# Optimization experiments

Hardware: AMD Instinct MI355X
Metric: run time of the kernel (lower is better)

## Reference

```python
import jax, jax.numpy as jnp
import numpy as np

N = 16384            # number of input vectors
CODEBOOK_SIZE = 8192  # M
DIM = 256             # dim_feature
BETA = 0.25           # commitment_weight


def setup_inputs() -> dict:
    key = jax.random.key(0)
    kx, ke = jax.random.split(key)
    x = jax.random.normal(kx, (N, DIM), dtype=jnp.float32)
    # kaiming-uniform-style init for the codebook
    bound = float(np.sqrt(3.0 / DIM))
    embeddings = jax.random.uniform(ke, (CODEBOOK_SIZE, DIM), dtype=jnp.float32,
                                    minval=-bound, maxval=bound)
    return {"x": x, "embeddings": embeddings}


def reference(x, embeddings):
    # l2_dist: sqrt(sum((x_i - e_j)^2)) computed via the GEMM expansion
    x2 = jnp.sum(x * x, axis=1, keepdims=True)               # (N, 1)
    e2 = jnp.sum(embeddings * embeddings, axis=1)            # (M,)
    d2 = x2 + e2[None, :] - 2.0 * (x @ embeddings.T)         # (N, M)
    dist = jnp.sqrt(jnp.maximum(d2, 0.0))
    # deterministic gumbel_sample path (training eval / stochastic=False):
    # argmax of logits = -dist  <=>  argmin of dist
    ind = jnp.argmin(dist, axis=1)                           # (N,)
    quantized = embeddings[ind]                              # one_hot @ embeddings
    # commitment loss: beta * ||x_q - sg(x)||^2 (docstring)
    commit_loss = BETA * jnp.mean((quantized - jax.lax.stop_gradient(x)) ** 2)
    # straight-through estimator
    quantized_st = x + jax.lax.stop_gradient(quantized - x)
    # perplexity from per-code counts (one-hot scatter)
    counts = jnp.zeros((CODEBOOK_SIZE,), jnp.float32).at[ind].add(1.0)
    probs = counts / counts.sum()
    perplexity = jnp.exp(-jnp.sum(probs * jnp.log(probs + 1e-10)))
    return quantized_st, ind, commit_loss, perplexity
```

## Files before the change

kernel.cpp:

```cpp
#include <hip/hip_runtime.h>
#include <stdint.h>


#define N_VEC 16384
#define M_CODES 8192
#define DIM 256
#define BETA 0.25f

#define NSLICE 4
#define SLICE_CODES 2048
#define BM 256
#define BN 256
#define NPART 8

#define XSLOT 32768
#define ESLOT 32768
#define EBASE (3 * XSLOT)
#define LDS_TOTAL (3 * XSLOT + 2 * ESLOT)
#define NSTEPS 64

typedef __attribute__((ext_vector_type(4))) float f32x4;
typedef __attribute__((ext_vector_type(8))) __bf16 bf16x8;

__device__ __forceinline__ void gll16(const void* g, const void* lds_p) {
    __builtin_amdgcn_global_load_lds(
        (const __attribute__((address_space(1))) uint32_t*)(uintptr_t)g,
        (__attribute__((address_space(3))) uint32_t*)(uint32_t)(uintptr_t)lds_p,
        16, 0, 0);
}
#define SB0() __builtin_amdgcn_sched_barrier(0)

__device__ __forceinline__ ushort f2bf(float f) {
    uint32_t u = __float_as_uint(f);
    return (ushort)((u + 0x7FFFu + ((u >> 16) & 1u)) >> 16);
}
__device__ __forceinline__ float bf2f(ushort h) {
    return __uint_as_float(((uint32_t)h) << 16);
}

__global__ __launch_bounds__(256) void prep_kernel(
    const float* __restrict__ x, const float* __restrict__ emb,
    ushort* __restrict__ xh, ushort* __restrict__ xl,
    ushort* __restrict__ eh, ushort* __restrict__ el,
    float* __restrict__ e2, unsigned* __restrict__ counts,
    float* __restrict__ loss_acc) {
    if (blockIdx.x < 8) {
        int4 z = {0, 0, 0, 0};
        ((int4*)counts)[blockIdx.x * 256 + threadIdx.x] = z;
        if (blockIdx.x == 0 && threadIdx.x == 0) *loss_acc = 0.0f;
    }
    const int wave = threadIdx.x >> 6;
    const int lane = threadIdx.x & 63;
    const int row = blockIdx.x * 4 + wave;

    const float* src;
    ushort* ph;
    ushort* pl;
    bool is_e;
    int er = row - N_VEC;
    if (row < N_VEC) {
        src = x + (size_t)row * DIM;
        ph = xh + (size_t)row * DIM;
        pl = xl + (size_t)row * DIM;
        is_e = false;
    } else {
        src = emb + (size_t)er * DIM;
        ph = eh + (size_t)er * DIM;
        pl = el + (size_t)er * DIM;
        is_e = true;
    }
    float4 v = *(const float4*)(src + lane * 4);
    ushort h0 = f2bf(v.x), h1 = f2bf(v.y), h2 = f2bf(v.z), h3 = f2bf(v.w);
    ushort l0 = f2bf(v.x - bf2f(h0)), l1 = f2bf(v.y - bf2f(h1));
    ushort l2 = f2bf(v.z - bf2f(h2)), l3 = f2bf(v.w - bf2f(h3));
    *(ushort4*)(ph + lane * 4) = make_ushort4(h0, h1, h2, h3);
    *(ushort4*)(pl + lane * 4) = make_ushort4(l0, l1, l2, l3);
    if (is_e) {
        float s = v.x * v.x + v.y * v.y + v.z * v.z + v.w * v.w;
        #pragma unroll
        for (int off = 32; off; off >>= 1) s += __shfl_xor(s, off);
        if (lane == 0) e2[er] = s;
    }
}

__global__ __launch_bounds__(512, 1) void vq_mfma_kernel(
    const ushort* __restrict__ xh, const ushort* __restrict__ xl,
    const ushort* __restrict__ eh, const ushort* __restrict__ el,
    const float* __restrict__ e2g, unsigned long long* __restrict__ partials) {
    extern __shared__ char lds[];

    const int t = threadIdx.x;
    const int lane = t & 63;
    const int wv = t >> 6;
    const int lane15 = lane & 15;
    const int l16 = lane >> 4;

    const int rt = blockIdx.x & 63;
    const int slice = blockIdx.x >> 6;
    const int row0 = rt * BM;
    const int cslice0 = slice * SLICE_CODES;

    const int wr0 = (wv & 3) * 64;
    const int wch = wv >> 2;

    const int swz = ((l16 ^ (lane15 >> 1)) & 3) << 4;
    const int byteA0 = (wr0 + lane15) * 64 + swz;
    const int byteB0 = (wch * 128 + lane15) * 64 + swz;

    const int s0 = wv * 128 + lane;
    const int s1 = s0 + 64;
    const int r0s = s0 >> 2, r1s = s1 >> 2;
    const int c0s = ((s0 & 3) ^ ((s0 >> 3) & 3)) << 3;
    const int c1s = ((s1 & 3) ^ ((s1 >> 3) & 3)) << 3;

    const ushort* pxh_a = xh + (size_t)(row0 + r0s) * DIM + c0s;
    const ushort* pxh_b = xh + (size_t)(row0 + r1s) * DIM + c1s;
    const ushort* pxl_a = xl + (size_t)(row0 + r0s) * DIM + c0s;
    const ushort* pxl_b = xl + (size_t)(row0 + r1s) * DIM + c1s;
    const ushort* peh_a = eh + (size_t)(cslice0 + r0s) * DIM + c0s;
    const ushort* peh_b = eh + (size_t)(cslice0 + r1s) * DIM + c1s;
    const ushort* pel_a = el + (size_t)(cslice0 + r0s) * DIM + c0s;
    const ushort* pel_b = el + (size_t)(cslice0 + r1s) * DIM + c1s;
    const int wdst = wv * 2048;

    auto stage_X = [&](int slot, int s) {
        char* b = lds + slot * XSLOT + wdst;
        const int xo = (s & 7) * 32;
        gll16(pxh_a + xo, b);
        gll16(pxh_b + xo, b + 1024);
        gll16(pxl_a + xo, b + 16384);
        gll16(pxl_b + xo, b + 16384 + 1024);
    };
    auto stage_E = [&](int slot, int s) {
        char* b = lds + EBASE + slot * ESLOT + wdst;
        const size_t eo = ((size_t)(s >> 3) << 16) + (s & 7) * 32;
        gll16(peh_a + eo, b);
        gll16(peh_b + eo, b + 1024);
        gll16(pel_a + eo, b + 16384);
        gll16(pel_b + eo, b + 16384 + 1024);
    };

    float best[16];
    int bidx[16];
    #pragma unroll
    for (int s = 0; s < 16; ++s) { best[s] = __uint_as_float(0x7f800000u); bidx[s] = 0; }

    f32x4 acc[4][8];
    #pragma unroll
    for (int fi = 0; fi < 4; ++fi)
        #pragma unroll
        for (int fj = 0; fj < 8; ++fj) acc[fi][fj] = (f32x4){0.f, 0.f, 0.f, 0.f};

    float e2r[8];

    stage_X(0, 0); SB0();
    stage_E(0, 0); SB0();
    stage_X(1, 1); SB0();

    int xsl = 0;
    for (int s = 0; s < NSTEPS; ++s) {
        if (s == NSTEPS - 1) {
            asm volatile("s_waitcnt vmcnt(0)" ::: "memory");
        } else {
            asm volatile("s_waitcnt vmcnt(4)" ::: "memory");
        }
        __builtin_amdgcn_s_barrier();
        SB0();
        if ((s & 7) == 0) {
            const int ct = s >> 3;
            const int cb = cslice0 + ct * BN + wch * 128 + lane15;
            #pragma unroll
            for (int fj = 0; fj < 8; ++fj) e2r[fj] = e2g[cb + fj * 16];
            SB0();
        }
        if (s + 1 < NSTEPS) { stage_E((s + 1) & 1, s + 1); SB0(); }
        if (s + 2 < NSTEPS) { stage_X((xsl >= 1) ? xsl - 1 : 2, s + 2); SB0(); }

        const char* lbX = lds + xsl * XSLOT;
        const char* lbE = lds + EBASE + (s & 1) * ESLOT;
        bf16x8 ah[4], alo[4];
        #pragma unroll
        for (int f = 0; f < 4; ++f) {
            ah[f] = *(const bf16x8*)(lbX + byteA0 + f * 1024);
            alo[f] = *(const bf16x8*)(lbX + 16384 + byteA0 + f * 1024);
        }
        __builtin_amdgcn_s_setprio(1);
        #pragma unroll
        for (int fj = 0; fj < 8; ++fj) {
            bf16x8 bh = *(const bf16x8*)(lbE + byteB0 + fj * 1024);
            bf16x8 blo = *(const bf16x8*)(lbE + 16384 + byteB0 + fj * 1024);
            #pragma unroll
            for (int fi = 0; fi < 4; ++fi)
                acc[fi][fj] = __builtin_amdgcn_mfma_f32_16x16x32_bf16(
                    ah[fi], bh, acc[fi][fj], 0, 0, 0);
            #pragma unroll
            for (int fi = 0; fi < 4; ++fi)
                acc[fi][fj] = __builtin_amdgcn_mfma_f32_16x16x32_bf16(
                    ah[fi], blo, acc[fi][fj], 0, 0, 0);
            #pragma unroll
            for (int fi = 0; fi < 4; ++fi)
                acc[fi][fj] = __builtin_amdgcn_mfma_f32_16x16x32_bf16(
                    alo[fi], bh, acc[fi][fj], 0, 0, 0);
        }
        __builtin_amdgcn_s_setprio(0);
        xsl = (xsl == 2) ? 0 : xsl + 1;

        if ((s & 7) == 7) {
            const int ct = s >> 3;
            const int cb = cslice0 + ct * BN + wch * 128 + lane15;
            #pragma unroll
            for (int fj = 0; fj < 8; ++fj) {
                const int c = cb + fj * 16;
                #pragma unroll
                for (int fi = 0; fi < 4; ++fi)
                    #pragma unroll
                    for (int r = 0; r < 4; ++r) {
                        float sc = e2r[fj] - 2.0f * acc[fi][fj][r];
                        const int slot = fi * 4 + r;
                        if (sc < best[slot]) { best[slot] = sc; bidx[slot] = c; }
                    }
            }
            #pragma unroll
            for (int fi = 0; fi < 4; ++fi)
                #pragma unroll
                for (int fj = 0; fj < 8; ++fj)
                    acc[fi][fj] = (f32x4){0.f, 0.f, 0.f, 0.f};
        }
    }

    #pragma unroll
    for (int slot = 0; slot < 16; ++slot) {
        float v = best[slot];
        int ix = bidx[slot];
        #pragma unroll
        for (int off = 1; off < 16; off <<= 1) {
            float v2 = __shfl_xor(v, off);
            int ix2 = __shfl_xor(ix, off);
            if (v2 < v || (v2 == v && ix2 < ix)) { v = v2; ix = ix2; }
        }
        if (lane15 == 0) {
            int fi = slot >> 2, r = slot & 3;
            int row = row0 + wr0 + fi * 16 + l16 * 4 + r;
            uint32_t u = __float_as_uint(v);
            uint32_t ord = (u & 0x80000000u) ? ~u : (u | 0x80000000u);
            partials[(size_t)(slice * 2 + wch) * N_VEC + row] =
                ((unsigned long long)ord << 32) | (unsigned)ix;
        }
    }
}

__global__ __launch_bounds__(256) void finish_kernel(
    const float* __restrict__ x, const float* __restrict__ emb,
    const unsigned long long* __restrict__ partials,
    float* __restrict__ out_ind, float* __restrict__ out_q,
    unsigned* __restrict__ counts, float* __restrict__ loss_acc) {
    __shared__ float partial[4];
    const int wave = threadIdx.x >> 6;
    const int lane = threadIdx.x & 63;
    const int row = blockIdx.x * 4 + wave;

    unsigned long long m = ~0ull;
    if (lane < NPART) m = partials[(size_t)lane * N_VEC + row];
    #pragma unroll
    for (int off = 1; off < NPART; off <<= 1) {
        unsigned long long v = __shfl_xor(m, off);
        if (v < m) m = v;
    }
    m = __shfl(m, 0);
    const int ix = (int)(unsigned)(m & 0xFFFFFFFFull);

    float4 q = *(const float4*)(emb + (size_t)ix * DIM + lane * 4);
    float4 xv = *(const float4*)(x + (size_t)row * DIM + lane * 4);
    *(float4*)(out_q + (size_t)row * DIM + lane * 4) = q;
    float dx = q.x - xv.x, dy = q.y - xv.y, dz = q.z - xv.z, dw = q.w - xv.w;
    float s = dx * dx + dy * dy + dz * dz + dw * dw;
    #pragma unroll
    for (int off = 32; off; off >>= 1) s += __shfl_xor(s, off);
    if (lane == 0) {
        out_ind[row] = (float)ix;
        atomicAdd(&counts[ix], 1u);
        partial[wave] = s;
    }
    __syncthreads();
    if (threadIdx.x == 0)
        atomicAdd(loss_acc, partial[0] + partial[1] + partial[2] + partial[3]);
}

__global__ __launch_bounds__(256) void finalize_kernel(
    const unsigned* __restrict__ counts, const float* __restrict__ loss_acc,
    float* __restrict__ out_scalars) {
    __shared__ float red[256];
    float h = 0.0f;
    for (int c = threadIdx.x; c < M_CODES; c += 256) {
        float p = (float)counts[c] * (1.0f / (float)N_VEC);
        h += p * logf(p + 1e-10f);
    }
    red[threadIdx.x] = h;
    __syncthreads();
    for (int s = 128; s; s >>= 1) {
        if (threadIdx.x < s) red[threadIdx.x] += red[threadIdx.x + s];
        __syncthreads();
    }
    if (threadIdx.x == 0) {
        out_scalars[0] = BETA * loss_acc[0] / (float)(N_VEC * DIM);
        out_scalars[1] = expf(-red[0]);
    }
}

extern "C" void kernel_launch(void* const* d_in, const int* in_sizes, int n_in,
                              void* d_out, int out_size, void* d_ws, size_t ws_size,
                              hipStream_t stream) {
    const float* x = (const float*)d_in[0];
    const float* emb = (const float*)d_in[1];

    float* out = (float*)d_out;
    float* out_q = out;
    float* out_ind = out + (size_t)N_VEC * DIM;
    float* out_scalars = out_ind + N_VEC;

    ushort* xh = (ushort*)out;
    ushort* xl = xh + (size_t)N_VEC * DIM;

    char* wp = (char*)d_ws;
    ushort* eh = (ushort*)wp;  wp += (size_t)M_CODES * DIM * 2;
    ushort* el = (ushort*)wp;  wp += (size_t)M_CODES * DIM * 2;
    float* e2 = (float*)wp;    wp += (size_t)M_CODES * 4;
    unsigned long long* partials = (unsigned long long*)wp;
    wp += (size_t)NPART * N_VEC * 8;
    unsigned* counts = (unsigned*)wp; wp += (size_t)M_CODES * 4;
    float* loss_acc = (float*)wp;

    prep_kernel<<<(N_VEC + M_CODES) / 4, 256, 0, stream>>>(x, emb, xh, xl, eh, el,
                                                           e2, counts, loss_acc);

    hipFuncSetAttribute((const void*)vq_mfma_kernel,
                        hipFuncAttributeMaxDynamicSharedMemorySize, LDS_TOTAL);
    vq_mfma_kernel<<<(N_VEC / BM) * NSLICE, 512, LDS_TOTAL, stream>>>(
        xh, xl, eh, el, e2, partials);

    finish_kernel<<<N_VEC / 4, 256, 0, stream>>>(x, emb, partials, out_ind, out_q,
                                                 counts, loss_acc);
    finalize_kernel<<<1, 256, 0, stream>>>(counts, loss_acc, out_scalars);
}
```

Baseline: 240.5 us.

## Shrink GEMM tiles to 128x128 with 256-thread blocks and simple double buffering

Reduces the block tile from 256x256 with 8 waves to 128x128 with 4 waves, and allows two blocks per CU. The separate triple-buffered X and double-buffered E staging becomes one combined double buffer, and each step now waits for all loads to finish. Smaller tiles cut LDS use and register pressure to allow more occupancy. In exchange, each loaded byte feeds fewer MFMAs, global traffic roughly doubles, and load latency is less well hidden because of the vmcnt(0) wait.

```diff
diff --git a/kernel.cpp b/kernel.cpp
--- a/kernel.cpp
+++ b/kernel.cpp
@@ -9,15 +9,13 @@
 
 #define NSLICE 4
 #define SLICE_CODES 2048
-#define BM 256
-#define BN 256
+#define BM 128
+#define BN 128
 #define NPART 8
 
-#define XSLOT 32768
-#define ESLOT 32768
-#define EBASE (3 * XSLOT)
-#define LDS_TOTAL (3 * XSLOT + 2 * ESLOT)
-#define NSTEPS 64
+#define BUFBYTES 32768
+#define LDS_TOTAL (2 * BUFBYTES)
+#define NSTEPS 128
 
 typedef __attribute__((ext_vector_type(4))) float f32x4;
 typedef __attribute__((ext_vector_type(8))) __bf16 bf16x8;
@@ -83,7 +81,7 @@
     }
 }
 
-__global__ __launch_bounds__(512, 1) void vq_mfma_kernel(
+__global__ __launch_bounds__(256, 2) void vq_mfma_kernel(
     const ushort* __restrict__ xh, const ushort* __restrict__ xl,
     const ushort* __restrict__ eh, const ushort* __restrict__ el,
     const float* __restrict__ e2g, unsigned long long* __restrict__ partials) {
@@ -95,17 +93,17 @@
     const int lane15 = lane & 15;
     const int l16 = lane >> 4;
 
-    const int rt = blockIdx.x & 63;
-    const int slice = blockIdx.x >> 6;
+    const int rt = blockIdx.x & 127;
+    const int slice = blockIdx.x >> 7;
     const int row0 = rt * BM;
     const int cslice0 = slice * SLICE_CODES;
 
-    const int wr0 = (wv & 3) * 64;
-    const int wch = wv >> 2;
+    const int wr0 = (wv & 1) * 64;
+    const int wch = wv >> 1;
 
     const int swz = ((l16 ^ (lane15 >> 1)) & 3) << 4;
     const int byteA0 = (wr0 + lane15) * 64 + swz;
-    const int byteB0 = (wch * 128 + lane15) * 64 + swz;
+    const int byteB0 = (wch * 64 + lane15) * 64 + swz;
 
     const int s0 = wv * 128 + lane;
     const int s1 = s0 + 64;
@@ -123,21 +121,18 @@
     const ushort* pel_b = el + (size_t)(cslice0 + r1s) * DIM + c1s;
     const int wdst = wv * 2048;
 
-    auto stage_X = [&](int slot, int s) {
-        char* b = lds + slot * XSLOT + wdst;
+    auto stage = [&](int bufOff, int s) {
+        char* b = lds + bufOff + wdst;
         const int xo = (s & 7) * 32;
+        const size_t eo = ((size_t)(s >> 3) << 15) + (s & 7) * 32;
         gll16(pxh_a + xo, b);
         gll16(pxh_b + xo, b + 1024);
-        gll16(pxl_a + xo, b + 16384);
-        gll16(pxl_b + xo, b + 16384 + 1024);
-    };
-    auto stage_E = [&](int slot, int s) {
-        char* b = lds + EBASE + slot * ESLOT + wdst;
-        const size_t eo = ((size_t)(s >> 3) << 16) + (s & 7) * 32;
-        gll16(peh_a + eo, b);
-        gll16(peh_b + eo, b + 1024);
-        gll16(pel_a + eo, b + 16384);
-        gll16(pel_b + eo, b + 16384 + 1024);
+        gll16(pxl_a + xo, b + 8192);
+        gll16(pxl_b + xo, b + 8192 + 1024);
+        gll16(peh_a + eo, b + 16384);
+        gll16(peh_b + eo, b + 16384 + 1024);
+        gll16(pel_a + eo, b + 24576);
+        gll16(pel_b + eo, b + 24576 + 1024);
     };
 
     float best[16];
@@ -145,50 +140,40 @@
     #pragma unroll
     for (int s = 0; s < 16; ++s) { best[s] = __uint_as_float(0x7f800000u); bidx[s] = 0; }
 
-    f32x4 acc[4][8];
+    f32x4 acc[4][4];
     #pragma unroll
     for (int fi = 0; fi < 4; ++fi)
         #pragma unroll
-        for (int fj = 0; fj < 8; ++fj) acc[fi][fj] = (f32x4){0.f, 0.f, 0.f, 0.f};
-
-    float e2r[8];
-
-    stage_X(0, 0); SB0();
-    stage_E(0, 0); SB0();
-    stage_X(1, 1); SB0();
-
-    int xsl = 0;
+        for (int fj = 0; fj < 4; ++fj) acc[fi][fj] = (f32x4){0.f, 0.f, 0.f, 0.f};
+
+    float e2r[4];
+
+    stage(0, 0); SB0();
+
     for (int s = 0; s < NSTEPS; ++s) {
-        if (s == NSTEPS - 1) {
-            asm volatile("s_waitcnt vmcnt(0)" ::: "memory");
-        } else {
-            asm volatile("s_waitcnt vmcnt(4)" ::: "memory");
-        }
+        asm volatile("s_waitcnt vmcnt(0)" ::: "memory");
         __builtin_amdgcn_s_barrier();
         SB0();
+        if (s + 1 < NSTEPS) { stage(((s + 1) & 1) * BUFBYTES, s + 1); SB0(); }
         if ((s & 7) == 0) {
-            const int ct = s >> 3;
-            const int cb = cslice0 + ct * BN + wch * 128 + lane15;
-            #pragma unroll
-            for (int fj = 0; fj < 8; ++fj) e2r[fj] = e2g[cb + fj * 16];
+            const int cb = cslice0 + (s >> 3) * BN + wch * 64 + lane15;
+            #pragma unroll
+            for (int fj = 0; fj < 4; ++fj) e2r[fj] = e2g[cb + fj * 16];
             SB0();
         }
-        if (s + 1 < NSTEPS) { stage_E((s + 1) & 1, s + 1); SB0(); }
-        if (s + 2 < NSTEPS) { stage_X((xsl >= 1) ? xsl - 1 : 2, s + 2); SB0(); }
-
-        const char* lbX = lds + xsl * XSLOT;
-        const char* lbE = lds + EBASE + (s & 1) * ESLOT;
+
+        const char* lb = lds + (s & 1) * BUFBYTES;
         bf16x8 ah[4], alo[4];
         #pragma unroll
         for (int f = 0; f < 4; ++f) {
-            ah[f] = *(const bf16x8*)(lbX + byteA0 + f * 1024);
-            alo[f] = *(const bf16x8*)(lbX + 16384 + byteA0 + f * 1024);
+            ah[f] = *(const bf16x8*)(lb + byteA0 + f * 1024);
+            alo[f] = *(const bf16x8*)(lb + 8192 + byteA0 + f * 1024);
         }
         __builtin_amdgcn_s_setprio(1);
         #pragma unroll
-        for (int fj = 0; fj < 8; ++fj) {
-            bf16x8 bh = *(const bf16x8*)(lbE + byteB0 + fj * 1024);
-            bf16x8 blo = *(const bf16x8*)(lbE + 16384 + byteB0 + fj * 1024);
+        for (int fj = 0; fj < 4; ++fj) {
+            bf16x8 bh = *(const bf16x8*)(lb + 16384 + byteB0 + fj * 1024);
+            bf16x8 blo = *(const bf16x8*)(lb + 24576 + byteB0 + fj * 1024);
             #pragma unroll
             for (int fi = 0; fi < 4; ++fi)
                 acc[fi][fj] = __builtin_amdgcn_mfma_f32_16x16x32_bf16(
@@ -203,13 +188,12 @@
                     alo[fi], bh, acc[fi][fj], 0, 0, 0);
         }
         __builtin_amdgcn_s_setprio(0);
-        xsl = (xsl == 2) ? 0 : xsl + 1;
 
         if ((s & 7) == 7) {
             const int ct = s >> 3;
-            const int cb = cslice0 + ct * BN + wch * 128 + lane15;
-            #pragma unroll
-            for (int fj = 0; fj < 8; ++fj) {
+            const int cb = cslice0 + ct * BN + wch * 64 + lane15;
+            #pragma unroll
+            for (int fj = 0; fj < 4; ++fj) {
                 const int c = cb + fj * 16;
                 #pragma unroll
                 for (int fi = 0; fi < 4; ++fi)
@@ -223,7 +207,7 @@
             #pragma unroll
             for (int fi = 0; fi < 4; ++fi)
                 #pragma unroll
-                for (int fj = 0; fj < 8; ++fj)
+                for (int fj = 0; fj < 4; ++fj)
                     acc[fi][fj] = (f32x4){0.f, 0.f, 0.f, 0.f};
         }
     }
@@ -335,7 +319,7 @@
 
     hipFuncSetAttribute((const void*)vq_mfma_kernel,
                         hipFuncAttributeMaxDynamicSharedMemorySize, LDS_TOTAL);
-    vq_mfma_kernel<<<(N_VEC / BM) * NSLICE, 512, LDS_TOTAL, stream>>>(
+    vq_mfma_kernel<<<(N_VEC / BM) * NSLICE, 256, LDS_TOTAL, stream>>>(
         xh, xl, eh, el, e2, partials);
 
     finish_kernel<<<N_VEC / 4, 256, 0, stream>>>(x, emb, partials, out_ind, out_q,
```

New measurement: 265.1 us. 10.2% more time.

## Switch VQ distance GEMM to 32x32x16 MFMA with hand-scheduled LDS reads

Applied to the files above, without the earlier changes.

Replaces the 16x16x32 bf16 MFMA tiling with 32x32x16 MFMAs, so each wave holds 2x4 accumulators of 16 floats and issues fewer, larger matrix instructions. LDS fragment loads become explicit ds_read_b128 with manual lgkmcnt waits, interleaved with the MFMA groups so B reads overlap compute. The per-row argmin epilogue is rebuilt around cross-lane shuffle, min and ballot reductions into a single packed 64-bit best per lane, which removes the 16-slot best arrays and the final shuffle reduction. Risks include register pressure from the larger accumulators, a heavier epilogue every 8 steps, and changed tie-breaking order.

```diff
diff --git a/kernel.cpp b/kernel.cpp
--- a/kernel.cpp
+++ b/kernel.cpp
@@ -19,7 +19,8 @@
 #define LDS_TOTAL (3 * XSLOT + 2 * ESLOT)
 #define NSTEPS 64
 
-typedef __attribute__((ext_vector_type(4))) float f32x4;
+typedef __attribute__((ext_vector_type(16))) float f32x16;
+typedef __attribute__((ext_vector_type(4))) int i32x4;
 typedef __attribute__((ext_vector_type(8))) __bf16 bf16x8;
 
 __device__ __forceinline__ void gll16(const void* g, const void* lds_p) {
@@ -29,6 +30,9 @@
         16, 0, 0);
 }
 #define SB0() __builtin_amdgcn_sched_barrier(0)
+#define DSR(DST, ADDR, OFF) \
+    asm volatile("ds_read_b128 %0, %1 offset:" #OFF : "=v"(DST) : "v"(ADDR))
+#define LGKM(N) asm volatile("s_waitcnt lgkmcnt(" #N ")" ::: "memory")
 
 __device__ __forceinline__ ushort f2bf(float f) {
     uint32_t u = __float_as_uint(f);
@@ -92,8 +96,8 @@
     const int t = threadIdx.x;
     const int lane = t & 63;
     const int wv = t >> 6;
-    const int lane15 = lane & 15;
-    const int l16 = lane >> 4;
+    const int l31 = lane & 31;
+    const int lh5 = lane >> 5;
 
     const int rt = blockIdx.x & 63;
     const int slice = blockIdx.x >> 6;
@@ -103,9 +107,14 @@
     const int wr0 = (wv & 3) * 64;
     const int wch = wv >> 2;
 
-    const int swz = ((l16 ^ (lane15 >> 1)) & 3) << 4;
-    const int byteA0 = (wr0 + lane15) * 64 + swz;
-    const int byteB0 = (wch * 128 + lane15) * 64 + swz;
+    const int rowA = wr0 + l31;
+    const int swzA = (rowA >> 1) & 3;
+    const int byteA_k0 = rowA * 64 + (((0 + lh5) ^ swzA) << 4);
+    const int byteA_k1 = rowA * 64 + (((2 + lh5) ^ swzA) << 4);
+    const int rowB = wch * 128 + l31;
+    const int swzB = (rowB >> 1) & 3;
+    const int byteB_k0 = rowB * 64 + (((0 + lh5) ^ swzB) << 4);
+    const int byteB_k1 = rowB * 64 + (((2 + lh5) ^ swzB) << 4);
 
     const int s0 = wv * 128 + lane;
     const int s1 = s0 + 64;
@@ -140,18 +149,38 @@
         gll16(pel_b + eo, b + 16384 + 1024);
     };
 
-    float best[16];
-    int bidx[16];
+    unsigned long long bestp = ~0ull;
+
+    f32x16 acc[2][4];
+    const f32x16 ZF = {};
     #pragma unroll
-    for (int s = 0; s < 16; ++s) { best[s] = __uint_as_float(0x7f800000u); bidx[s] = 0; }
-
-    f32x4 acc[4][8];
-    #pragma unroll
-    for (int fi = 0; fi < 4; ++fi)
+    for (int fi = 0; fi < 2; ++fi)
         #pragma unroll
-        for (int fj = 0; fj < 8; ++fj) acc[fi][fj] = (f32x4){0.f, 0.f, 0.f, 0.f};
-
-    float e2r[8];
+        for (int fj = 0; fj < 4; ++fj) acc[fi][fj] = ZF;
+
+    float e2r[4];
+
+#define MFMA32(A, B, C) __builtin_amdgcn_mfma_f32_32x32x16_bf16(A, B, C, 0, 0, 0)
+#define HHLH(FJ, B0R, B1R) do {                                  \
+    bf16x8 bh0_ = __builtin_bit_cast(bf16x8, B0R);               \
+    bf16x8 bh1_ = __builtin_bit_cast(bf16x8, B1R);               \
+    acc[0][FJ] = MFMA32(A00, bh0_, acc[0][FJ]);                  \
+    acc[1][FJ] = MFMA32(A10, bh0_, acc[1][FJ]);                  \
+    acc[0][FJ] = MFMA32(A01, bh1_, acc[0][FJ]);                  \
+    acc[1][FJ] = MFMA32(A11, bh1_, acc[1][FJ]);                  \
+    acc[0][FJ] = MFMA32(L00, bh0_, acc[0][FJ]);                  \
+    acc[1][FJ] = MFMA32(L10, bh0_, acc[1][FJ]);                  \
+    acc[0][FJ] = MFMA32(L01, bh1_, acc[0][FJ]);                  \
+    acc[1][FJ] = MFMA32(L11, bh1_, acc[1][FJ]);                  \
+    } while (0)
+#define HLB(FJ, B0R, B1R) do {                                   \
+    bf16x8 bl0_ = __builtin_bit_cast(bf16x8, B0R);               \
+    bf16x8 bl1_ = __builtin_bit_cast(bf16x8, B1R);               \
+    acc[0][FJ] = MFMA32(A00, bl0_, acc[0][FJ]);                  \
+    acc[1][FJ] = MFMA32(A10, bl0_, acc[1][FJ]);                  \
+    acc[0][FJ] = MFMA32(A01, bl1_, acc[0][FJ]);                  \
+    acc[1][FJ] = MFMA32(A11, bl1_, acc[1][FJ]);                  \
+    } while (0)
 
     stage_X(0, 0); SB0();
     stage_E(0, 0); SB0();
@@ -167,85 +196,113 @@
         __builtin_amdgcn_s_barrier();
         SB0();
         if ((s & 7) == 0) {
-            const int ct = s >> 3;
-            const int cb = cslice0 + ct * BN + wch * 128 + lane15;
+            const int cb = cslice0 + (s >> 3) * BN + wch * 128 + l31;
             #pragma unroll
-            for (int fj = 0; fj < 8; ++fj) e2r[fj] = e2g[cb + fj * 16];
+            for (int fj = 0; fj < 4; ++fj) e2r[fj] = e2g[cb + fj * 32];
             SB0();
         }
         if (s + 1 < NSTEPS) { stage_E((s + 1) & 1, s + 1); SB0(); }
         if (s + 2 < NSTEPS) { stage_X((xsl >= 1) ? xsl - 1 : 2, s + 2); SB0(); }
 
-        const char* lbX = lds + xsl * XSLOT;
-        const char* lbE = lds + EBASE + (s & 1) * ESLOT;
-        bf16x8 ah[4], alo[4];
-        #pragma unroll
-        for (int f = 0; f < 4; ++f) {
-            ah[f] = *(const bf16x8*)(lbX + byteA0 + f * 1024);
-            alo[f] = *(const bf16x8*)(lbX + 16384 + byteA0 + f * 1024);
-        }
+        const uint32_t ax = (uint32_t)(uintptr_t)(lds + xsl * XSLOT);
+        const uint32_t bx = (uint32_t)(uintptr_t)(lds + EBASE + (s & 1) * ESLOT);
+        const uint32_t vAk0 = ax + (uint32_t)byteA_k0;
+        const uint32_t vAk1 = ax + (uint32_t)byteA_k1;
+        const uint32_t vBk0 = bx + (uint32_t)byteB_k0;
+        const uint32_t vBk1 = bx + (uint32_t)byteB_k1;
+
+        i32x4 a00, a01, a10, a11, q00, q01, q10, q11, b0, b1, p0, p1;
+        DSR(a00, vAk0, 0);     DSR(a01, vAk1, 0);
+        DSR(a10, vAk0, 2048);  DSR(a11, vAk1, 2048);
+        DSR(q00, vAk0, 16384); DSR(q01, vAk1, 16384);
+        DSR(q10, vAk0, 18432); DSR(q11, vAk1, 18432);
+        DSR(b0, vBk0, 0);      DSR(b1, vBk1, 0);
         __builtin_amdgcn_s_setprio(1);
-        #pragma unroll
-        for (int fj = 0; fj < 8; ++fj) {
-            bf16x8 bh = *(const bf16x8*)(lbE + byteB0 + fj * 1024);
-            bf16x8 blo = *(const bf16x8*)(lbE + 16384 + byteB0 + fj * 1024);
-            #pragma unroll
-            for (int fi = 0; fi < 4; ++fi)
-                acc[fi][fj] = __builtin_amdgcn_mfma_f32_16x16x32_bf16(
-                    ah[fi], bh, acc[fi][fj], 0, 0, 0);
-            #pragma unroll
-            for (int fi = 0; fi < 4; ++fi)
-                acc[fi][fj] = __builtin_amdgcn_mfma_f32_16x16x32_bf16(
-                    ah[fi], blo, acc[fi][fj], 0, 0, 0);
-            #pragma unroll
-            for (int fi = 0; fi < 4; ++fi)
-                acc[fi][fj] = __builtin_amdgcn_mfma_f32_16x16x32_bf16(
-                    alo[fi], bh, acc[fi][fj], 0, 0, 0);
-        }
+        DSR(p0, vBk0, 2048);   DSR(p1, vBk1, 2048);
+        LGKM(2); SB0();
+
+        bf16x8 A00 = __builtin_bit_cast(bf16x8, a00);
+        bf16x8 A01 = __builtin_bit_cast(bf16x8, a01);
+        bf16x8 A10 = __builtin_bit_cast(bf16x8, a10);
+        bf16x8 A11 = __builtin_bit_cast(bf16x8, a11);
+        bf16x8 L00 = __builtin_bit_cast(bf16x8, q00);
+        bf16x8 L01 = __builtin_bit_cast(bf16x8, q01);
+        bf16x8 L10 = __builtin_bit_cast(bf16x8, q10);
+        bf16x8 L11 = __builtin_bit_cast(bf16x8, q11);
+
+        HHLH(0, b0, b1);
+        DSR(b0, vBk0, 4096);  DSR(b1, vBk1, 4096);
+        LGKM(2); SB0();
+        HHLH(1, p0, p1);
+        DSR(p0, vBk0, 6144);  DSR(p1, vBk1, 6144);
+        LGKM(2); SB0();
+        HHLH(2, b0, b1);
+        LGKM(0); SB0();
+        HHLH(3, p0, p1);
+
+        DSR(b0, vBk0, 16384); DSR(b1, vBk1, 16384);
+        DSR(p0, vBk0, 18432); DSR(p1, vBk1, 18432);
+        LGKM(2); SB0();
+        HLB(0, b0, b1);
+        DSR(b0, vBk0, 20480); DSR(b1, vBk1, 20480);
+        LGKM(2); SB0();
+        HLB(1, p0, p1);
+        DSR(p0, vBk0, 22528); DSR(p1, vBk1, 22528);
+        LGKM(2); SB0();
+        HLB(2, b0, b1);
+        LGKM(0); SB0();
+        HLB(3, p0, p1);
         __builtin_amdgcn_s_setprio(0);
         xsl = (xsl == 2) ? 0 : xsl + 1;
 
         if ((s & 7) == 7) {
-            const int ct = s >> 3;
-            const int cb = cslice0 + ct * BN + wch * 128 + lane15;
+            const int cb = cslice0 + (s >> 3) * BN + wch * 128;
             #pragma unroll
-            for (int fj = 0; fj < 8; ++fj) {
-                const int c = cb + fj * 16;
+            for (int fi = 0; fi < 2; ++fi)
                 #pragma unroll
-                for (int fi = 0; fi < 4; ++fi)
+                for (int reg = 0; reg < 16; ++reg) {
+                    float m = e2r[0] - 2.0f * acc[fi][0][reg];
+                    int cf = 0;
+                    float s1 = e2r[1] - 2.0f * acc[fi][1][reg];
+                    if (s1 < m) { m = s1; cf = 1; }
+                    float s2 = e2r[2] - 2.0f * acc[fi][2][reg];
+                    if (s2 < m) { m = s2; cf = 2; }
+                    float s3 = e2r[3] - 2.0f * acc[fi][3][reg];
+                    if (s3 < m) { m = s3; cf = 3; }
+                    float mr = m;
                     #pragma unroll
-                    for (int r = 0; r < 4; ++r) {
-                        float sc = e2r[fj] - 2.0f * acc[fi][fj][r];
-                        const int slot = fi * 4 + r;
-                        if (sc < best[slot]) { best[slot] = sc; bidx[slot] = c; }
+                    for (int off = 1; off < 32; off <<= 1)
+                        mr = fminf(mr, __shfl_xor(mr, off));
+                    unsigned long long bal = __ballot(m == mr);
+                    unsigned mask32 = (unsigned)(bal >> (lane & 32));
+                    int win = __ffs((int)mask32) - 1;
+                    int cfw = __shfl(cf, win | (lane & 32));
+                    int col = cb + cfw * 32 + win;
+                    if (l31 == ((fi << 4) | ((reg >> 2) << 2) | (reg & 3))) {
+                        uint32_t u = __float_as_uint(mr);
+                        uint32_t ord = (u & 0x80000000u) ? ~u : (u | 0x80000000u);
+                        unsigned long long pk =
+                            ((unsigned long long)ord << 32) | (unsigned)col;
+                        if (pk < bestp) bestp = pk;
                     }
-            }
+                }
             #pragma unroll
-            for (int fi = 0; fi < 4; ++fi)
+            for (int fi = 0; fi < 2; ++fi)
                 #pragma unroll
-                for (int fj = 0; fj < 8; ++fj)
-                    acc[fi][fj] = (f32x4){0.f, 0.f, 0.f, 0.f};
+                for (int fj = 0; fj < 4; ++fj) acc[fi][fj] = ZF;
         }
     }
-
-    #pragma unroll
-    for (int slot = 0; slot < 16; ++slot) {
-        float v = best[slot];
-        int ix = bidx[slot];
-        #pragma unroll
-        for (int off = 1; off < 16; off <<= 1) {
-            float v2 = __shfl_xor(v, off);
-            int ix2 = __shfl_xor(ix, off);
-            if (v2 < v || (v2 == v && ix2 < ix)) { v = v2; ix = ix2; }
-        }
-        if (lane15 == 0) {
-            int fi = slot >> 2, r = slot & 3;
-            int row = row0 + wr0 + fi * 16 + l16 * 4 + r;
-            uint32_t u = __float_as_uint(v);
-            uint32_t ord = (u & 0x80000000u) ? ~u : (u | 0x80000000u);
-            partials[(size_t)(slice * 2 + wch) * N_VEC + row] =
-                ((unsigned long long)ord << 32) | (unsigned)ix;
-        }
+#undef HHLH
+#undef HLB
+#undef MFMA32
+
+    {
+        const int fi_o = (lane >> 4) & 1;
+        const int rhi = (lane >> 2) & 3;
+        const int rlo = lane & 3;
+        const int half = lane >> 5;
+        const int row = row0 + wr0 + fi_o * 32 + rlo + 8 * rhi + 4 * half;
+        partials[(size_t)(slice * 2 + wch) * N_VEC + row] = bestp;
     }
 }
 
```

After: 302.7 us. 25.9% more time.

## Restructure GEMM main loop into 8-phase interleaved loads with LDS best tracking

Applied to the files above, without the earlier changes.

The main loop drops the triple/double X/E LDS buffering in favour of a two-buffer scheme. Each step is split into eight phases, and each phase issues one global-to-LDS load alongside the B-fragment reads and an MFMA burst, using barriers and explicit ds_read_b128 waits. Per-row argmin state moves from registers into LDS, updated after every code tile via a shuffle reduction, and the two wave-column halves are merged in-kernel, which halves the partials written (NPART 8→4). e2 is staged in LDS once per block. The aim is to free registers and finely overlap memory with MFMA, at the cost of many more barriers and per-tile reduction work.

```diff
diff --git a/kernel.cpp b/kernel.cpp
--- a/kernel.cpp
+++ b/kernel.cpp
@@ -11,15 +11,16 @@
 #define SLICE_CODES 2048
 #define BM 256
 #define BN 256
-#define NPART 8
-
-#define XSLOT 32768
-#define ESLOT 32768
-#define EBASE (3 * XSLOT)
-#define LDS_TOTAL (3 * XSLOT + 2 * ESLOT)
+#define NPART 4
+
+#define BUF_BYTES 65536
+#define E2_OFF (2 * BUF_BYTES)
+#define BEST_OFF (E2_OFF + 8192)
+#define LDS_TOTAL (BEST_OFF + 4096)
 #define NSTEPS 64
 
 typedef __attribute__((ext_vector_type(4))) float f32x4;
+typedef __attribute__((ext_vector_type(4))) int i32x4;
 typedef __attribute__((ext_vector_type(8))) __bf16 bf16x8;
 
 __device__ __forceinline__ void gll16(const void* g, const void* lds_p) {
@@ -29,6 +30,9 @@
         16, 0, 0);
 }
 #define SB0() __builtin_amdgcn_sched_barrier(0)
+#define DSR(DST, ADDR, OFF) \
+    asm volatile("ds_read_b128 %0, %1 offset:" #OFF : "=v"(DST) : "v"(ADDR))
+#define LGKM(N) asm volatile("s_waitcnt lgkmcnt(" #N ")" ::: "memory")
 
 __device__ __forceinline__ ushort f2bf(float f) {
     uint32_t u = __float_as_uint(f);
@@ -121,29 +125,14 @@
     const ushort* peh_b = eh + (size_t)(cslice0 + r1s) * DIM + c1s;
     const ushort* pel_a = el + (size_t)(cslice0 + r0s) * DIM + c0s;
     const ushort* pel_b = el + (size_t)(cslice0 + r1s) * DIM + c1s;
-    const int wdst = wv * 2048;
-
-    auto stage_X = [&](int slot, int s) {
-        char* b = lds + slot * XSLOT + wdst;
-        const int xo = (s & 7) * 32;
-        gll16(pxh_a + xo, b);
-        gll16(pxh_b + xo, b + 1024);
-        gll16(pxl_a + xo, b + 16384);
-        gll16(pxl_b + xo, b + 16384 + 1024);
-    };
-    auto stage_E = [&](int slot, int s) {
-        char* b = lds + EBASE + slot * ESLOT + wdst;
-        const size_t eo = ((size_t)(s >> 3) << 16) + (s & 7) * 32;
-        gll16(peh_a + eo, b);
-        gll16(peh_b + eo, b + 1024);
-        gll16(pel_a + eo, b + 16384);
-        gll16(pel_b + eo, b + 16384 + 1024);
-    };
-
-    float best[16];
-    int bidx[16];
+
+    float* e2s = (float*)(lds + E2_OFF);
+    unsigned long long* bestU = (unsigned long long*)(lds + BEST_OFF);
+
     #pragma unroll
-    for (int s = 0; s < 16; ++s) { best[s] = __uint_as_float(0x7f800000u); bidx[s] = 0; }
+    for (int i = 0; i < 4; ++i) e2s[i * 512 + t] = e2g[cslice0 + i * 512 + t];
+    bestU[t] = ~0ull;
+    __syncthreads();
 
     f32x4 acc[4][8];
     #pragma unroll
@@ -151,75 +140,114 @@
         #pragma unroll
         for (int fj = 0; fj < 8; ++fj) acc[fi][fj] = (f32x4){0.f, 0.f, 0.f, 0.f};
 
-    float e2r[8];
-
-    stage_X(0, 0); SB0();
-    stage_E(0, 0); SB0();
-    stage_X(1, 1); SB0();
-
-    int xsl = 0;
+#define BURST(P) do {                                                        \
+    bf16x8 BH_ = __builtin_bit_cast(bf16x8, bh_);                            \
+    bf16x8 BL_ = __builtin_bit_cast(bf16x8, bl_);                            \
+    _Pragma("unroll") for (int fi_ = 0; fi_ < 4; ++fi_)                      \
+        acc[fi_][P] = __builtin_amdgcn_mfma_f32_16x16x32_bf16(               \
+            __builtin_bit_cast(bf16x8, Ah[fi_]), BH_, acc[fi_][P], 0, 0, 0); \
+    _Pragma("unroll") for (int fi_ = 0; fi_ < 4; ++fi_)                      \
+        acc[fi_][P] = __builtin_amdgcn_mfma_f32_16x16x32_bf16(               \
+            __builtin_bit_cast(bf16x8, Ah[fi_]), BL_, acc[fi_][P], 0, 0, 0); \
+    _Pragma("unroll") for (int fi_ = 0; fi_ < 4; ++fi_)                      \
+        acc[fi_][P] = __builtin_amdgcn_mfma_f32_16x16x32_bf16(               \
+            __builtin_bit_cast(bf16x8, Al[fi_]), BH_, acc[fi_][P], 0, 0, 0); \
+} while (0)
+
+#define PHASE(P, OH, OL, ...) do {                                           \
+    DSR(bh_, vB, OH); DSR(bl_, vB, OL);                                      \
+    if (sn < NSTEPS) { __VA_ARGS__; }                                        \
+    __builtin_amdgcn_s_barrier();                                            \
+    LGKM(0); SB0();                                                          \
+    __builtin_amdgcn_s_setprio(1);                                           \
+    BURST(P);                                                                \
+    __builtin_amdgcn_s_setprio(0);                                           \
+    __builtin_amdgcn_s_barrier();                                            \
+} while (0)
+
+    {
+        char* b = lds + wv * 2048;
+        gll16(pxh_a, b);
+        gll16(pxh_b, b + 1024);
+        gll16(pxl_a, b + 16384);
+        gll16(pxl_b, b + 16384 + 1024);
+        gll16(peh_a, b + 32768);
+        gll16(peh_b, b + 32768 + 1024);
+        gll16(pel_a, b + 49152);
+        gll16(pel_b, b + 49152 + 1024);
+        SB0();
+    }
+
     for (int s = 0; s < NSTEPS; ++s) {
-        if (s == NSTEPS - 1) {
-            asm volatile("s_waitcnt vmcnt(0)" ::: "memory");
-        } else {
-            asm volatile("s_waitcnt vmcnt(4)" ::: "memory");
-        }
+        asm volatile("s_waitcnt vmcnt(0)" ::: "memory");
         __builtin_amdgcn_s_barrier();
         SB0();
-        if ((s & 7) == 0) {
+
+        const int sn = s + 1;
+        const int xo = (sn & 7) * 32;
+        const size_t eo = ((size_t)(sn >> 3) << 16) + (sn & 7) * 32;
+        char* wb = lds + (sn & 1) * BUF_BYTES + wv * 2048;
+        const char* rb = lds + (s & 1) * BUF_BYTES;
+        const uint32_t vA = (uint32_t)(uintptr_t)rb + (uint32_t)byteA0;
+        const uint32_t vB = (uint32_t)(uintptr_t)rb + 32768u + (uint32_t)byteB0;
+
+        i32x4 Ah[4], Al[4], bh_, bl_;
+
+        DSR(Ah[0], vA, 0);     DSR(Ah[1], vA, 1024);
+        DSR(Ah[2], vA, 2048);  DSR(Ah[3], vA, 3072);
+        DSR(Al[0], vA, 16384); DSR(Al[1], vA, 17408);
+        DSR(Al[2], vA, 18432); DSR(Al[3], vA, 19456);
+        DSR(bh_, vB, 0);       DSR(bl_, vB, 16384);
+        if (sn < NSTEPS) { gll16(pxh_a + xo, wb); }
+        LGKM(0); SB0();
+        __builtin_amdgcn_s_setprio(1);
+        BURST(0);
+        __builtin_amdgcn_s_setprio(0);
+        __builtin_amdgcn_s_barrier();
+
+        PHASE(1, 1024, 17408, gll16(pxh_b + xo, wb + 1024));
+        PHASE(2, 2048, 18432, gll16(pxl_a + xo, wb + 16384));
+        PHASE(3, 3072, 19456, gll16(pxl_b + xo, wb + 16384 + 1024));
+        PHASE(4, 4096, 20480, gll16(peh_a + eo, wb + 32768));
+        PHASE(5, 5120, 21504, gll16(peh_b + eo, wb + 32768 + 1024));
+        PHASE(6, 6144, 22528, gll16(pel_a + eo, wb + 49152));
+        PHASE(7, 7168, 23552, gll16(pel_b + eo, wb + 49152 + 1024));
+
+        if ((s & 7) == 7) {
             const int ct = s >> 3;
-            const int cb = cslice0 + ct * BN + wch * 128 + lane15;
+            float e2v[8];
             #pragma unroll
-            for (int fj = 0; fj < 8; ++fj) e2r[fj] = e2g[cb + fj * 16];
-            SB0();
-        }
-        if (s + 1 < NSTEPS) { stage_E((s + 1) & 1, s + 1); SB0(); }
-        if (s + 2 < NSTEPS) { stage_X((xsl >= 1) ? xsl - 1 : 2, s + 2); SB0(); }
-
-        const char* lbX = lds + xsl * XSLOT;
-        const char* lbE = lds + EBASE + (s & 1) * ESLOT;
-        bf16x8 ah[4], alo[4];
-        #pragma unroll
-        for (int f = 0; f < 4; ++f) {
-            ah[f] = *(const bf16x8*)(lbX + byteA0 + f * 1024);
-            alo[f] = *(const bf16x8*)(lbX + 16384 + byteA0 + f * 1024);
-        }
-        __builtin_amdgcn_s_setprio(1);
-        #pragma unroll
-        for (int fj = 0; fj < 8; ++fj) {
-            bf16x8 bh = *(const bf16x8*)(lbE + byteB0 + fj * 1024);
-            bf16x8 blo = *(const bf16x8*)(lbE + 16384 + byteB0 + fj * 1024);
+            for (int fj = 0; fj < 8; ++fj)
+                e2v[fj] = e2s[ct * 256 + wch * 128 + fj * 16 + lane15];
+            const int cb = cslice0 + ct * 256 + wch * 128 + lane15;
             #pragma unroll
             for (int fi = 0; fi < 4; ++fi)
-                acc[fi][fj] = __builtin_amdgcn_mfma_f32_16x16x32_bf16(
-                    ah[fi], bh, acc[fi][fj], 0, 0, 0);
-            #pragma unroll
-            for (int fi = 0; fi < 4; ++fi)
-                acc[fi][fj] = __builtin_amdgcn_mfma_f32_16x16x32_bf16(
-                    ah[fi], blo, acc[fi][fj], 0, 0, 0);
-            #pragma unroll
-            for (int fi = 0; fi < 4; ++fi)
-                acc[fi][fj] = __builtin_amdgcn_mfma_f32_16x16x32_bf16(
-                    alo[fi], bh, acc[fi][fj], 0, 0, 0);
-        }
-        __builtin_amdgcn_s_setprio(0);
-        xsl = (xsl == 2) ? 0 : xsl + 1;
-
-        if ((s & 7) == 7) {
-            const int ct = s >> 3;
-            const int cb = cslice0 + ct * BN + wch * 128 + lane15;
-            #pragma unroll
-            for (int fj = 0; fj < 8; ++fj) {
-                const int c = cb + fj * 16;
                 #pragma unroll
-                for (int fi = 0; fi < 4; ++fi)
+                for (int r = 0; r < 4; ++r) {
+                    float m = e2v[0] - 2.0f * acc[fi][0][r];
+                    int c = cb;
                     #pragma unroll
-                    for (int r = 0; r < 4; ++r) {
-                        float sc = e2r[fj] - 2.0f * acc[fi][fj][r];
-                        const int slot = fi * 4 + r;
-                        if (sc < best[slot]) { best[slot] = sc; bidx[slot] = c; }
+                    for (int fj = 1; fj < 8; ++fj) {
+                        float sc = e2v[fj] - 2.0f * acc[fi][fj][r];
+                        if (sc < m) { m = sc; c = cb + fj * 16; }
                     }
-            }
+                    #pragma unroll
+                    for (int off = 1; off < 16; off <<= 1) {
+                        float v2 = __shfl_xor(m, off);
+                        int c2 = __shfl_xor(c, off);
+                        if (v2 < m || (v2 == m && c2 < c)) { m = v2; c = c2; }
+                    }
+                    if (lane15 == 0) {
+                        int rowL = wr0 + fi * 16 + l16 * 4 + r;
+                        uint32_t u = __float_as_uint(m);
+                        uint32_t ord =
+                            (u & 0x80000000u) ? ~u : (u | 0x80000000u);
+                        unsigned long long pk =
+                            ((unsigned long long)ord << 32) | (unsigned)c;
+                        unsigned long long* e = &bestU[wch * 256 + rowL];
+                        if (pk < *e) *e = pk;
+                    }
+                }
             #pragma unroll
             for (int fi = 0; fi < 4; ++fi)
                 #pragma unroll
@@ -227,25 +255,15 @@
                     acc[fi][fj] = (f32x4){0.f, 0.f, 0.f, 0.f};
         }
     }
-
-    #pragma unroll
-    for (int slot = 0; slot < 16; ++slot) {
-        float v = best[slot];
-        int ix = bidx[slot];
-        #pragma unroll
-        for (int off = 1; off < 16; off <<= 1) {
-            float v2 = __shfl_xor(v, off);
-            int ix2 = __shfl_xor(ix, off);
-            if (v2 < v || (v2 == v && ix2 < ix)) { v = v2; ix = ix2; }
-        }
-        if (lane15 == 0) {
-            int fi = slot >> 2, r = slot & 3;
-            int row = row0 + wr0 + fi * 16 + l16 * 4 + r;
-            uint32_t u = __float_as_uint(v);
-            uint32_t ord = (u & 0x80000000u) ? ~u : (u | 0x80000000u);
-            partials[(size_t)(slice * 2 + wch) * N_VEC + row] =
-                ((unsigned long long)ord << 32) | (unsigned)ix;
-        }
+#undef PHASE
+#undef BURST
+
+    __syncthreads();
+    if (t < 256) {
+        unsigned long long m = bestU[t];
+        unsigned long long m2 = bestU[256 + t];
+        if (m2 < m) m = m2;
+        partials[(size_t)slice * N_VEC + row0 + t] = m;
     }
 }
 
```

Measured after the change: 279.0 us. 16.0% more time.
